# Kernel optimization log

Hardware: AMD Instinct MI355X
Metric: run time of the kernel (lower is better)

## Reference

```python
import jax, jax.numpy as jnp
import numpy as np

D_MODEL = 1024
D_STATE = 16
D_CONV = 4
EXPAND = 2
D_INNER = EXPAND * D_MODEL
DT_RANK = D_MODEL // 16  # ceil(1024/16) = 64
BSZ = 2
SEQ = 1024


def _silu(x):
    return x * jax.nn.sigmoid(x)


def _mamba(x, in_proj, conv_w, conv_b, x_proj, dt_w, dt_b, A_log, Dp, out_proj):
    """Single-direction Mamba block. x: (B, L, d_model)."""
    Bb, Ll, _ = x.shape
    xz = jnp.einsum('bld,ed->ble', x, in_proj)          # (B,L,2*d_inner)
    xi, z = jnp.split(xz, 2, axis=-1)                   # (B,L,d_inner)
    # depthwise causal conv1d over L (kernel d_conv)
    xp = jnp.pad(xi, ((0, 0), (D_CONV - 1, 0), (0, 0)))
    xc = conv_b + sum(conv_w[:, k] * xp[:, k:k + Ll, :] for k in range(D_CONV))
    xc = _silu(xc)                                      # (B,L,d_inner)
    dbl = jnp.einsum('ble,fe->blf', xc, x_proj)         # (B,L,dt_rank+2*d_state)
    dt, Bm, Cm = jnp.split(dbl, [DT_RANK, DT_RANK + D_STATE], axis=-1)
    delta = jax.nn.softplus(jnp.einsum('blr,er->ble', dt, dt_w) + dt_b)  # (B,L,d_inner)
    A = -jnp.exp(A_log)                                 # (d_inner,d_state)
    dA = jnp.exp(delta[..., None] * A)                  # (B,L,E,N)
    dBu = (delta * xc)[..., None] * Bm[:, :, None, :]   # (B,L,E,N)
    def step(h, t):
        dA_t, dBu_t, C_t = t
        h = dA_t * h + dBu_t                            # (B,E,N)
        return h, jnp.einsum('ben,bn->be', h, C_t)
    h0 = jnp.zeros((Bb, D_INNER, D_STATE), x.dtype)
    _, ys = jax.lax.scan(step, h0, (dA.transpose(1, 0, 2, 3),
                                    dBu.transpose(1, 0, 2, 3),
                                    Cm.transpose(1, 0, 2)))
    y = ys.transpose(1, 0, 2) + xc * Dp                 # skip connection
    y = y * _silu(z)                                    # gate
    return jnp.einsum('ble,de->bld', y, out_proj)


def setup_inputs() -> dict:
    key = jax.random.key(0)
    ks = jax.random.split(key, 4)
    def nrm(k, shape, s=0.02):
        return s * jax.random.normal(k, shape, dtype=jnp.float32)
    def mamba_params(kb):
        k = jax.random.split(kb, 6)
        return dict(
            in_proj=nrm(k[0], (2 * D_INNER, D_MODEL)),
            conv_w=nrm(k[1], (D_INNER, D_CONV), 0.2),
            conv_b=jnp.zeros((D_INNER,), jnp.float32),
            x_proj=nrm(k[2], (DT_RANK + 2 * D_STATE, D_INNER)),
            dt_w=nrm(k[3], (D_INNER, DT_RANK), 0.1),
            dt_b=nrm(k[4], (D_INNER,), 0.5) - 4.0,  # softplus -> dt ~ 0.018
            A_log=jnp.log(jnp.broadcast_to(jnp.arange(1, D_STATE + 1, dtype=jnp.float32), (D_INNER, D_STATE))),
            D=jnp.ones((D_INNER,), jnp.float32),
            out_proj=nrm(k[5], (D_MODEL, D_INNER)),
        )
    inp = {'x': jax.random.normal(ks[2], (BSZ, SEQ, D_MODEL), dtype=jnp.float32)}
    for name, p in (('fwd', mamba_params(ks[0])), ('bwd', mamba_params(ks[1]))):
        for kk, v in p.items():
            inp[f'{name}_{kk}'] = v
    inp['merge_w'] = nrm(ks[3], (D_MODEL, 2 * D_MODEL))
    return inp


def reference(x,
              fwd_in_proj, fwd_conv_w, fwd_conv_b, fwd_x_proj, fwd_dt_w, fwd_dt_b,
              fwd_A_log, fwd_D, fwd_out_proj,
              bwd_in_proj, bwd_conv_w, bwd_conv_b, bwd_x_proj, bwd_dt_w, bwd_dt_b,
              bwd_A_log, bwd_D, bwd_out_proj,
              merge_w):
    f = _mamba(x, fwd_in_proj, fwd_conv_w, fwd_conv_b, fwd_x_proj, fwd_dt_w,
               fwd_dt_b, fwd_A_log, fwd_D, fwd_out_proj)
    b = _mamba(jnp.flip(x, 1), bwd_in_proj, bwd_conv_w, bwd_conv_b, bwd_x_proj,
               bwd_dt_w, bwd_dt_b, bwd_A_log, bwd_D, bwd_out_proj)
    b = jnp.flip(b, 1)
    return jnp.einsum('blf,df->bld', jnp.concatenate([f, b], axis=-1), merge_w)
```

## Files before the change

kernel.cpp:

```cpp
#include <hip/hip_runtime.h>
#include <math.h>

#define BSZ 2
#define SEQ 1024
#define DM  1024
#define DI  2048
#define DS  16
#define DC  4
#define DR  64
#define NDBL 96
#define NC  32
#define LC  32
#define MM  (BSZ * SEQ)

typedef unsigned short u16;
typedef __bf16 bf16x8 __attribute__((ext_vector_type(8)));
typedef float  f32x4  __attribute__((ext_vector_type(4)));

constexpr int N4_X   = MM * DM / 4;
constexpr int N4_MW  = DM * 2 * DM / 4;
constexpr int N4_IN  = 2 * DI * DM / 4;
constexpr int N4_XP  = NDBL * DI / 4;
constexpr int N4_DT  = DI * DR / 4;
constexpr int N4_OUT = DM * DI / 4;
constexpr int N4_TOTAL = N4_X + N4_MW + 2 * (N4_IN + N4_XP + N4_DT + N4_OUT);
constexpr size_t O_XP  = (size_t)2 * DI * DM;
constexpr size_t O_DT  = O_XP + (size_t)NDBL * DI;
constexpr size_t O_OUT = O_DT + (size_t)DI * DR;
constexpr size_t WBF_SZ = O_OUT + (size_t)DM * DI;

__device__ __forceinline__ u16 f2b(float f) {
    unsigned int u = __float_as_uint(f);
    unsigned int r = (u + 0x7fffu + ((u >> 16) & 1u)) >> 16;
    return (u16)r;
}
__device__ __forceinline__ float b2f(u16 h) {
    return __uint_as_float(((unsigned int)h) << 16);
}

__device__ __forceinline__ void stf(float* p, size_t i, float v) { p[i] = v; }
__device__ __forceinline__ void stf(u16* p, size_t i, float v)   { p[i] = f2b(v); }

__device__ __forceinline__ float fexp(float x)  { return __expf(x); }
__device__ __forceinline__ float frcp(float x)  { return __builtin_amdgcn_rcpf(x); }
__device__ __forceinline__ float silu_fast(float x) {
    return x * frcp(1.f + fexp(-x));
}
__device__ __forceinline__ float softplus_fast(float x) {
    return (x > 15.f) ? x : __logf(1.f + fexp(x));
}

__device__ __forceinline__ void async16(const u16* g, u16* l) {
    __builtin_amdgcn_global_load_lds(
        (const __attribute__((address_space(1))) void*)g,
        (__attribute__((address_space(3))) void*)l, 16, 0, 0);
}

__device__ __forceinline__ int lds_slot(int row, int j) {
    return row * 4 + ((j + (row >> 1)) & 3);
}

__device__ __forceinline__ void stage8f(const float* p, u16* d) {
    float4 v0 = *(const float4*)p;
    float4 v1 = *(const float4*)(p + 4);
    ushort4 a; a.x = f2b(v0.x); a.y = f2b(v0.y); a.z = f2b(v0.z); a.w = f2b(v0.w);
    ushort4 b; b.x = f2b(v1.x); b.y = f2b(v1.y); b.z = f2b(v1.z); b.w = f2b(v1.w);
    *(ushort4*)d = a;
    *(ushort4*)(d + 4) = b;
}

__global__ __launch_bounds__(256) void cvt_all_kernel(
    const float* __restrict__ s0, const float* __restrict__ s1,
    const float* __restrict__ s2, const float* __restrict__ s3,
    const float* __restrict__ s4, const float* __restrict__ s5,
    const float* __restrict__ s6, const float* __restrict__ s7,
    const float* __restrict__ s8, const float* __restrict__ s9,
    u16* __restrict__ d0, u16* __restrict__ d1, u16* __restrict__ d2,
    u16* __restrict__ d3, u16* __restrict__ d4, u16* __restrict__ d5,
    u16* __restrict__ d6, u16* __restrict__ d7, u16* __restrict__ d8,
    u16* __restrict__ d9)
{
    int i = blockIdx.x * 256 + threadIdx.x;
    const float* s; u16* d;
    if (i < N4_X) { s = s0; d = d0; }
    else if ((i -= N4_X) < N4_MW) { s = s1; d = d1; }
    else if ((i -= N4_MW) < N4_IN) { s = s2; d = d2; }
    else if ((i -= N4_IN) < N4_XP) { s = s3; d = d3; }
    else if ((i -= N4_XP) < N4_DT) { s = s4; d = d4; }
    else if ((i -= N4_DT) < N4_OUT) { s = s5; d = d5; }
    else if ((i -= N4_OUT) < N4_IN) { s = s6; d = d6; }
    else if ((i -= N4_IN) < N4_XP) { s = s7; d = d7; }
    else if ((i -= N4_XP) < N4_DT) { s = s8; d = d8; }
    else if ((i -= N4_DT) < N4_OUT) { s = s9; d = d9; }
    else return;
    float4 v = ((const float4*)s)[i];
    ushort4 o; o.x = f2b(v.x); o.y = f2b(v.y); o.z = f2b(v.z); o.w = f2b(v.w);
    ((ushort4*)d)[i] = o;
}

template <typename TA, typename TC, int ACT, bool DUAL, bool FLIP1, int NSPLIT, int BN>
__global__ __launch_bounds__(256) void mfma_gemm(
    const TA* __restrict__ A0, const TA* __restrict__ A1, int lda,
    const u16* __restrict__ W0, const u16* __restrict__ W1, int ldw,
    const float* __restrict__ bias0, const float* __restrict__ bias1,
    TC* __restrict__ C0, TC* __restrict__ C1, int ldc,
    int M, int N, int K)
{
    constexpr int NF = BN / 32;
    __shared__ u16 As[128 * 32];
    __shared__ u16 Ws[BN * 32];

    const int z = blockIdx.z;
    const int dir = DUAL ? (z / NSPLIT) : 0;
    const int split = z % NSPLIT;
    const TA* A = dir ? A1 : A0;
    const u16* W = dir ? W1 : W0;
    const float* bias = dir ? bias1 : bias0;
    TC* C = dir ? C1 : C0;
    if (NSPLIT > 1) C += (size_t)split * M * ldc;
    const int kseg = K / NSPLIT;
    const int kbeg = split * kseg, kend = kbeg + kseg;

    const int t = threadIdx.x;
    const int wave = t >> 6;
    const int lane = t & 63;
    const int wm = (wave & 1) * 64;
    const int wn = (wave >> 1) * (BN / 2);
    const int fm = lane & 15;
    const int q  = lane >> 4;
    const int m0 = blockIdx.y * 128;
    const int n0 = blockIdx.x * BN;

    f32x4 acc[4][NF] = {};

    for (int k0 = kbeg; k0 < kend; k0 += 32) {
        if constexpr (__is_same(TA, u16)) {
            #pragma unroll
            for (int p = 0; p < 2; p++) {
                int i = p * 256 + wave * 64 + lane;
                int r = i >> 2;
                int j = ((i & 3) - (r >> 1)) & 3;
                async16(A + (size_t)(m0 + r) * lda + k0 + j * 8,
                        &As[(size_t)(p * 256 + wave * 64) * 8]);
            }
        } else {
            #pragma unroll
            for (int p = 0; p < 2; p++) {
                int i = p * 256 + t;
                int r = i >> 2;
                int j = ((i & 3) - (r >> 1)) & 3;
                stage8f(A + (size_t)(m0 + r) * lda + k0 + j * 8, &As[(size_t)i * 8]);
            }
        }
        #pragma unroll
        for (int p = 0; p < BN / 64; p++) {
            int i = p * 256 + wave * 64 + lane;
            int r = i >> 2;
            int j = ((i & 3) - (r >> 1)) & 3;
            int gr = n0 + r;
            if (gr >= N) gr = N - 1;
            async16(W + (size_t)gr * ldw + k0 + j * 8,
                    &Ws[(size_t)(p * 256 + wave * 64) * 8]);
        }
        __syncthreads();

        bf16x8 af[4], wf[NF];
        #pragma unroll
        for (int mi = 0; mi < 4; mi++)
            af[mi] = *(const bf16x8*)&As[(size_t)lds_slot(wm + mi * 16 + fm, q) * 8];
        #pragma unroll
        for (int ni = 0; ni < NF; ni++)
            wf[ni] = *(const bf16x8*)&Ws[(size_t)lds_slot(wn + ni * 16 + fm, q) * 8];
        #pragma unroll
        for (int mi = 0; mi < 4; mi++)
            #pragma unroll
            for (int ni = 0; ni < NF; ni++)
                acc[mi][ni] = __builtin_amdgcn_mfma_f32_16x16x32_bf16(
                    af[mi], wf[ni], acc[mi][ni], 0, 0, 0);
        __syncthreads();
    }

    const int rb = q * 4;
    const int cc = fm;
    #pragma unroll
    for (int mi = 0; mi < 4; mi++) {
        #pragma unroll
        for (int r = 0; r < 4; r++) {
            int gm = m0 + wm + mi * 16 + rb + r;
            int om = gm;
            if (FLIP1 && dir == 1) {
                int bb = gm / SEQ, l = gm % SEQ;
                om = bb * SEQ + (SEQ - 1 - l);
            }
            #pragma unroll
            for (int ni = 0; ni < NF; ni++) {
                int gn = n0 + wn + ni * 16 + cc;
                if (gn < N) {
                    float v = acc[mi][ni][r];
                    if (ACT == 1) v = softplus_fast(v + bias[gn]);
                    stf(C, (size_t)om * ldc + gn, v);
                }
            }
        }
    }
}

__global__ __launch_bounds__(256) void combine_dbl_kernel(
    const float* __restrict__ par, float* __restrict__ dbl)
{
    int i4 = blockIdx.x * 256 + threadIdx.x;
    const int per = (MM * NDBL) / 4;
    int dir = (i4 >= per) ? 1 : 0;
    int j4 = i4 - dir * per;
    const float* p = par + (size_t)dir * 4 * MM * NDBL;
    f32x4 s = {0.f, 0.f, 0.f, 0.f};
    #pragma unroll
    for (int k = 0; k < 4; k++)
        s += *(const f32x4*)&p[(size_t)k * MM * NDBL + (size_t)j4 * 4];
    *(f32x4*)&dbl[(size_t)dir * MM * NDBL + (size_t)j4 * 4] = s;
}

__global__ __launch_bounds__(256) void combine_cat_kernel(
    const float* __restrict__ par, u16* __restrict__ cat)
{
    int i4 = blockIdx.x * 256 + threadIdx.x;
    const int per = (MM * DM) / 4;
    int dir = (i4 >= per) ? 1 : 0;
    int j4 = i4 - dir * per;
    const float* p0 = par + (size_t)dir * 2 * MM * DM;
    const float* p1 = p0 + (size_t)MM * DM;
    f32x4 a = *(const f32x4*)&p0[(size_t)j4 * 4];
    f32x4 b = *(const f32x4*)&p1[(size_t)j4 * 4];
    int m = j4 >> 8;
    int n4 = j4 & 255;
    ushort4 o;
    o.x = f2b(a[0] + b[0]); o.y = f2b(a[1] + b[1]);
    o.z = f2b(a[2] + b[2]); o.w = f2b(a[3] + b[3]);
    *(ushort4*)&cat[(size_t)m * 2 * DM + dir * DM + n4 * 4] = o;
}

__global__ __launch_bounds__(256) void combine_out_kernel(
    const float* __restrict__ p0, float* __restrict__ out)
{
    int i4 = blockIdx.x * 256 + threadIdx.x;
    const float* p1 = p0 + (size_t)MM * DM;
    f32x4 a = *(const f32x4*)&p0[(size_t)i4 * 4];
    f32x4 b = *(const f32x4*)&p1[(size_t)i4 * 4];
    *(f32x4*)&out[(size_t)i4 * 4] = a + b;
}

__global__ __launch_bounds__(256) void conv_silu_kernel(
    const float* __restrict__ xz,
    const float* __restrict__ cw0, const float* __restrict__ cw1,
    const float* __restrict__ cb0, const float* __restrict__ cb1,
    u16* __restrict__ xcb)
{
    int i4 = blockIdx.x * 256 + threadIdx.x;
    const int per = MM * DI / 4;
    int dir = (i4 >= per) ? 1 : 0;
    int rem = i4 - dir * per;
    int e4 = rem & (DI / 4 - 1);
    int bl = rem / (DI / 4);
    int l = bl & (SEQ - 1);
    int e = e4 * 4;
    const float* xz_d = xz + (size_t)dir * MM * 2 * DI;
    const float* cw = dir ? cw1 : cw0;
    const float* cb = dir ? cb1 : cb0;
    f32x4 cwv[4];
    #pragma unroll
    for (int i = 0; i < 4; i++) cwv[i] = *(const f32x4*)&cw[(e + i) * DC];
    f32x4 acc = *(const f32x4*)&cb[e];
    #pragma unroll
    for (int k = 0; k < DC; k++) {
        int ll = l + k - (DC - 1);
        if (ll >= 0) {
            f32x4 xv = *(const f32x4*)&xz_d[(size_t)(bl - l + ll) * (2 * DI) + e];
            #pragma unroll
            for (int i = 0; i < 4; i++) acc[i] += cwv[i][k] * xv[i];
        }
    }
    ushort4 o;
    #pragma unroll
    for (int i = 0; i < 4; i++) {
        float s = silu_fast(acc[i]);
        ((u16*)&o)[i] = f2b(s);
    }
    ((ushort4*)xcb)[(size_t)dir * per + rem] = o;
}

__global__ __launch_bounds__(256) void scan_pass1(
    const float* __restrict__ dbl,
    const u16*  __restrict__ xc,
    const u16*  __restrict__ delta,
    const float* __restrict__ Alog0, const float* __restrict__ Alog1,
    float* __restrict__ Pout, float* __restrict__ Qout)
{
    __shared__ float sB[LC][16];
    const int t = threadIdx.x;
    const int c = blockIdx.x;
    const int dir = blockIdx.z >> 1;
    const int b = blockIdx.z & 1;
    const int e = blockIdx.y * 256 + t;
    const int row0 = b * SEQ + c * LC;
    const float* dbl_d = dbl + (size_t)dir * MM * NDBL;
    const u16* xc_d = xc + (size_t)dir * MM * DI;
    const u16* delta_d = delta + (size_t)dir * MM * DI;
    const float* A_log = dir ? Alog1 : Alog0;
    float* P_d = Pout + (size_t)dir * BSZ * NC * DI * DS;
    float* Q_d = Qout + (size_t)dir * BSZ * NC * DI * DS;

    if (t < LC * 4) {
        int row = t >> 2, col = (t & 3) * 4;
        *(f32x4*)&sB[row][col] =
            *(const f32x4*)&dbl_d[(size_t)(row0 + row) * NDBL + DR + col];
    }

    f32x4 Aen[4], P[4], Q[4];
    #pragma unroll
    for (int g = 0; g < 4; g++) {
        f32x4 a = *(const f32x4*)&A_log[(size_t)e * DS + g * 4];
        #pragma unroll
        for (int j = 0; j < 4; j++) Aen[g][j] = -fexp(a[j]);
        P[g] = f32x4{1.f, 1.f, 1.f, 1.f};
        Q[g] = f32x4{0.f, 0.f, 0.f, 0.f};
    }
    __syncthreads();

    float dv = b2f(delta_d[(size_t)row0 * DI + e]);
    float xv = b2f(xc_d[(size_t)row0 * DI + e]);
    for (int i = 0; i < LC; i++) {
        int ip = (i + 1 < LC) ? (i + 1) : (LC - 1);
        float dvn = b2f(delta_d[(size_t)(row0 + ip) * DI + e]);
        float xvn = b2f(xc_d[(size_t)(row0 + ip) * DI + e]);
        float du = dv * xv;
        #pragma unroll
        for (int g = 0; g < 4; g++) {
            f32x4 Bv = *(const f32x4*)&sB[i][g * 4];
            #pragma unroll
            for (int j = 0; j < 4; j++) {
                float dA = fexp(dv * Aen[g][j]);
                P[g][j] *= dA;
                Q[g][j] = dA * Q[g][j] + du * Bv[j];
            }
        }
        dv = dvn; xv = xvn;
    }
    size_t base = ((size_t)(b * NC + c) * DI + e) * DS;
    #pragma unroll
    for (int g = 0; g < 4; g++) {
        *(f32x4*)&P_d[base + g * 4] = P[g];
        *(f32x4*)&Q_d[base + g * 4] = Q[g];
    }
}

__global__ __launch_bounds__(256) void scan_pass2(
    const float* __restrict__ P, const float* __restrict__ Q,
    float* __restrict__ H0)
{
    const int gid = blockIdx.x * 256 + threadIdx.x;
    const int dir = gid >> 16;
    const int loc = gid & 65535;
    const int b = loc >> 15;
    const int en = loc & (DI * DS - 1);
    size_t doff = (size_t)dir * BSZ * NC * DI * DS;
    float h = 0.f;
    for (int c = 0; c < NC; c++) {
        size_t idx = doff + ((size_t)(b * NC + c) * DI * DS) + en;
        H0[idx] = h;
        h = P[idx] * h + Q[idx];
    }
}

__global__ __launch_bounds__(256) void scan_pass3(
    const float* __restrict__ dbl,
    const u16*  __restrict__ xc,
    const float* __restrict__ xz,
    u16* delta_y,
    const float* __restrict__ Alog0, const float* __restrict__ Alog1,
    const float* __restrict__ Dp0, const float* __restrict__ Dp1,
    const float* __restrict__ H0)
{
    __shared__ float sBC[LC][32];
    const int t = threadIdx.x;
    const int c = blockIdx.x;
    const int dir = blockIdx.z >> 1;
    const int b = blockIdx.z & 1;
    const int e = blockIdx.y * 256 + t;
    const int row0 = b * SEQ + c * LC;
    const float* dbl_d = dbl + (size_t)dir * MM * NDBL;
    const u16* xc_d = xc + (size_t)dir * MM * DI;
    const float* xz_d = xz + (size_t)dir * MM * 2 * DI;
    u16* dy_d = delta_y + (size_t)dir * MM * DI;
    const float* A_log = dir ? Alog1 : Alog0;
    const float* Dp = dir ? Dp1 : Dp0;
    const float* H0_d = H0 + (size_t)dir * BSZ * NC * DI * DS;

    {
        int row = t >> 3, col = (t & 7) * 4;
        *(f32x4*)&sBC[row][col] =
            *(const f32x4*)&dbl_d[(size_t)(row0 + row) * NDBL + DR + col];
    }

    f32x4 Aen[4], h[4];
    size_t base = ((size_t)(b * NC + c) * DI + e) * DS;
    #pragma unroll
    for (int g = 0; g < 4; g++) {
        f32x4 a = *(const f32x4*)&A_log[(size_t)e * DS + g * 4];
        #pragma unroll
        for (int j = 0; j < 4; j++) Aen[g][j] = -fexp(a[j]);
        h[g] = *(const f32x4*)&H0_d[base + g * 4];
    }
    const float Dv = Dp[e];
    __syncthreads();

    float dv = b2f(dy_d[(size_t)row0 * DI + e]);
    float xv = b2f(xc_d[(size_t)row0 * DI + e]);
    float zv = xz_d[(size_t)row0 * (2 * DI) + DI + e];
    for (int i = 0; i < LC; i++) {
        int ip = (i + 1 < LC) ? (i + 1) : (LC - 1);
        float dvn = b2f(dy_d[(size_t)(row0 + ip) * DI + e]);
        float xvn = b2f(xc_d[(size_t)(row0 + ip) * DI + e]);
        float zvn = xz_d[(size_t)(row0 + ip) * (2 * DI) + DI + e];
        float du = dv * xv;
        f32x4 pv = {0.f, 0.f, 0.f, 0.f};
        #pragma unroll
        for (int g = 0; g < 4; g++) {
            f32x4 Bv = *(const f32x4*)&sBC[i][g * 4];
            f32x4 Cv = *(const f32x4*)&sBC[i][16 + g * 4];
            #pragma unroll
            for (int j = 0; j < 4; j++) {
                float dA = fexp(dv * Aen[g][j]);
                h[g][j] = dA * h[g][j] + du * Bv[j];
                pv[j] += h[g][j] * Cv[j];
            }
        }
        float p = pv[0] + pv[1] + pv[2] + pv[3];
        float y = (p + xv * Dv) * silu_fast(zv);
        dy_d[(size_t)(row0 + i) * DI + e] = f2b(y);
        dv = dvn; xv = xvn; zv = zvn;
    }
}

extern "C" void kernel_launch(void* const* d_in, const int* in_sizes, int n_in,
                              void* d_out, int out_size, void* d_ws, size_t ws_size,
                              hipStream_t stream)
{
    const float* x = (const float*)d_in[0];
    const float* in_p[2]  = {(const float*)d_in[1],  (const float*)d_in[10]};
    const float* conv_w[2]= {(const float*)d_in[2],  (const float*)d_in[11]};
    const float* conv_b[2]= {(const float*)d_in[3],  (const float*)d_in[12]};
    const float* x_p[2]   = {(const float*)d_in[4],  (const float*)d_in[13]};
    const float* dt_w[2]  = {(const float*)d_in[5],  (const float*)d_in[14]};
    const float* dt_b[2]  = {(const float*)d_in[6],  (const float*)d_in[15]};
    const float* A_log[2] = {(const float*)d_in[7],  (const float*)d_in[16]};
    const float* Dp[2]    = {(const float*)d_in[8],  (const float*)d_in[17]};
    const float* out_p[2] = {(const float*)d_in[9],  (const float*)d_in[18]};
    const float* merge_w  = (const float*)d_in[19];
    float* out = (float*)d_out;

    float* ws = (float*)d_ws;
    float* ws_xz  = ws;
    float* ws_dbl = ws_xz  + (size_t)2 * MM * 2 * DI;
    float* ws_P   = ws_dbl + (size_t)2 * MM * NDBL;
    float* ws_Q   = ws_P   + (size_t)2 * BSZ * NC * DI * DS;
    float* ws_H0  = ws_Q   + (size_t)2 * BSZ * NC * DI * DS;
    u16* ws_delta = (u16*)(ws_H0 + (size_t)2 * BSZ * NC * DI * DS);
    u16* ws_xcb   = ws_delta + (size_t)2 * MM * DI;
    u16* ws_cat   = ws_xcb   + (size_t)2 * MM * DI;
    u16* ws_xbf   = ws_cat   + (size_t)MM * 2 * DM;
    u16* wbf_mw   = ws_xbf   + (size_t)MM * DM;
    u16* wbf0     = wbf_mw   + (size_t)DM * 2 * DM;
    u16* wbf1     = wbf0     + WBF_SZ;
    float* ws_par = ws_P;

    cvt_all_kernel<<<(N4_TOTAL + 255) / 256, 256, 0, stream>>>(
        x, merge_w, in_p[0], x_p[0], dt_w[0], out_p[0],
        in_p[1], x_p[1], dt_w[1], out_p[1],
        ws_xbf, wbf_mw,
        wbf0, wbf0 + O_XP, wbf0 + O_DT, wbf0 + O_OUT,
        wbf1, wbf1 + O_XP, wbf1 + O_DT, wbf1 + O_OUT);

    mfma_gemm<u16, float, 0, true, true, 1, 128><<<dim3(32, 16, 2), 256, 0, stream>>>(
        ws_xbf, ws_xbf, DM, wbf0, wbf1, DM, nullptr, nullptr,
        ws_xz, ws_xz + (size_t)MM * 2 * DI, 2 * DI, MM, 2 * DI, DM);

    conv_silu_kernel<<<(2 * MM * DI / 4) / 256, 256, 0, stream>>>(
        ws_xz, conv_w[0], conv_w[1], conv_b[0], conv_b[1], ws_xcb);

    mfma_gemm<u16, float, 0, true, false, 4, 64><<<dim3(2, 16, 8), 256, 0, stream>>>(
        ws_xcb, ws_xcb + (size_t)MM * DI, DI,
        wbf0 + O_XP, wbf1 + O_XP, DI, nullptr, nullptr,
        ws_par, ws_par + (size_t)4 * MM * NDBL, NDBL, MM, NDBL, DI);
    combine_dbl_kernel<<<(2 * MM * NDBL / 4) / 256, 256, 0, stream>>>(ws_par, ws_dbl);

    mfma_gemm<float, u16, 1, true, false, 1, 64><<<dim3(32, 16, 2), 256, 0, stream>>>(
        ws_dbl, ws_dbl + (size_t)MM * NDBL, NDBL,
        wbf0 + O_DT, wbf1 + O_DT, DR, dt_b[0], dt_b[1],
        ws_delta, ws_delta + (size_t)MM * DI, DI, MM, DI, DR);

    {
        dim3 grid(NC, DI / 256, 2 * BSZ);
        scan_pass1<<<grid, 256, 0, stream>>>(ws_dbl, ws_xcb, ws_delta,
                                             A_log[0], A_log[1], ws_P, ws_Q);
        scan_pass2<<<(2 * BSZ * DI * DS) / 256, 256, 0, stream>>>(ws_P, ws_Q, ws_H0);
        scan_pass3<<<grid, 256, 0, stream>>>(ws_dbl, ws_xcb, ws_xz, ws_delta,
                                             A_log[0], A_log[1], Dp[0], Dp[1], ws_H0);
    }

    mfma_gemm<u16, float, 0, true, true, 2, 64><<<dim3(16, 16, 4), 256, 0, stream>>>(
        ws_delta, ws_delta + (size_t)MM * DI, DI,
        wbf0 + O_OUT, wbf1 + O_OUT, DI, nullptr, nullptr,
        ws_par, ws_par + (size_t)2 * MM * DM, DM, MM, DM, DI);
    combine_cat_kernel<<<(2 * MM * DM / 4) / 256, 256, 0, stream>>>(ws_par, ws_cat);

    mfma_gemm<u16, float, 0, false, false, 2, 64><<<dim3(16, 16, 2), 256, 0, stream>>>(
        ws_cat, ws_cat, 2 * DM, wbf_mw, wbf_mw, 2 * DM, nullptr, nullptr,
        ws_par, ws_par, DM, MM, DM, 2 * DM);
    combine_out_kernel<<<(MM * DM / 4) / 256, 256, 0, stream>>>(ws_par, out);
}
```

Baseline: 395.8 us.

## Double-buffer GEMM LDS, swizzle XCDs, store xz in bf16, drop out-proj split-K

The GEMM kernel gets double-buffered LDS tiles so the next K-slice loads while MFMAs run, plus an optional XCD-aware block swizzle. The in_proj output xz is now stored as bf16 instead of fp32, which cuts traffic in conv and scan_pass3. The out-proj GEMM loses its split-K and writes bf16 directly into the concat buffer, so combine_cat is no longer needed. The scan chunk count changes from 32x32 to 16x64, which trades parallelism for fewer chunk carries. The extra bf16 rounding of xz and z may lower accuracy slightly.

```diff
diff --git a/kernel.cpp b/kernel.cpp
--- a/kernel.cpp
+++ b/kernel.cpp
@@ -9,8 +9,8 @@
 #define DC  4
 #define DR  64
 #define NDBL 96
-#define NC  32
-#define LC  32
+#define NC  16
+#define LC  64
 #define MM  (BSZ * SEQ)
 
 typedef unsigned short u16;
@@ -58,6 +58,12 @@
 
 __device__ __forceinline__ int lds_slot(int row, int j) {
     return row * 4 + ((j + (row >> 1)) & 3);
+}
+
+__device__ __forceinline__ int xcd_swz(int flat, int nwg) {
+    int q = nwg >> 3, r = nwg & 7;
+    int x = flat & 7, i = flat >> 3;
+    return (x < r ? x * (q + 1) : r * (q + 1) + (x - r) * q) + i;
 }
 
 __device__ __forceinline__ void stage8f(const float* p, u16* d) {
@@ -98,7 +104,8 @@
     ((ushort4*)d)[i] = o;
 }
 
-template <typename TA, typename TC, int ACT, bool DUAL, bool FLIP1, int NSPLIT, int BN>
+template <typename TA, typename TC, int ACT, bool DUAL, bool FLIP1, int NSPLIT,
+          int BN, bool SWZ>
 __global__ __launch_bounds__(256) void mfma_gemm(
     const TA* __restrict__ A0, const TA* __restrict__ A1, int lda,
     const u16* __restrict__ W0, const u16* __restrict__ W1, int ldw,
@@ -107,10 +114,22 @@
     int M, int N, int K)
 {
     constexpr int NF = BN / 32;
-    __shared__ u16 As[128 * 32];
-    __shared__ u16 Ws[BN * 32];
-
-    const int z = blockIdx.z;
+    __shared__ u16 As[2][128 * 32];
+    __shared__ u16 Ws[2][BN * 32];
+
+    int bx = blockIdx.x, by = blockIdx.y, bz = blockIdx.z;
+    if (SWZ) {
+        const int gx = gridDim.x, gy = gridDim.y;
+        const int nwg = gx * gy * gridDim.z;
+        int flat = (blockIdx.z * gy + blockIdx.y) * gx + blockIdx.x;
+        flat = xcd_swz(flat, nwg);
+        bx = flat % gx;
+        int rest = flat / gx;
+        by = rest % gy;
+        bz = rest / gy;
+    }
+
+    const int z = bz;
     const int dir = DUAL ? (z / NSPLIT) : 0;
     const int split = z % NSPLIT;
     const TA* A = dir ? A1 : A0;
@@ -119,7 +138,8 @@
     TC* C = dir ? C1 : C0;
     if (NSPLIT > 1) C += (size_t)split * M * ldc;
     const int kseg = K / NSPLIT;
-    const int kbeg = split * kseg, kend = kbeg + kseg;
+    const int kbeg = split * kseg;
+    const int kiters = kseg / 32;
 
     const int t = threadIdx.x;
     const int wave = t >> 6;
@@ -128,12 +148,10 @@
     const int wn = (wave >> 1) * (BN / 2);
     const int fm = lane & 15;
     const int q  = lane >> 4;
-    const int m0 = blockIdx.y * 128;
-    const int n0 = blockIdx.x * BN;
-
-    f32x4 acc[4][NF] = {};
-
-    for (int k0 = kbeg; k0 < kend; k0 += 32) {
+    const int m0 = by * 128;
+    const int n0 = bx * BN;
+
+    auto stage_tile = [&](int k0, int b) {
         if constexpr (__is_same(TA, u16)) {
             #pragma unroll
             for (int p = 0; p < 2; p++) {
@@ -141,7 +159,7 @@
                 int r = i >> 2;
                 int j = ((i & 3) - (r >> 1)) & 3;
                 async16(A + (size_t)(m0 + r) * lda + k0 + j * 8,
-                        &As[(size_t)(p * 256 + wave * 64) * 8]);
+                        &As[b][(size_t)(p * 256 + wave * 64) * 8]);
             }
         } else {
             #pragma unroll
@@ -149,7 +167,8 @@
                 int i = p * 256 + t;
                 int r = i >> 2;
                 int j = ((i & 3) - (r >> 1)) & 3;
-                stage8f(A + (size_t)(m0 + r) * lda + k0 + j * 8, &As[(size_t)i * 8]);
+                stage8f(A + (size_t)(m0 + r) * lda + k0 + j * 8,
+                        &As[b][(size_t)i * 8]);
             }
         }
         #pragma unroll
@@ -160,23 +179,36 @@
             int gr = n0 + r;
             if (gr >= N) gr = N - 1;
             async16(W + (size_t)gr * ldw + k0 + j * 8,
-                    &Ws[(size_t)(p * 256 + wave * 64) * 8]);
-        }
-        __syncthreads();
+                    &Ws[b][(size_t)(p * 256 + wave * 64) * 8]);
+        }
+    };
+
+    f32x4 acc[4][NF] = {};
+
+    stage_tile(kbeg, 0);
+    __syncthreads();
+
+    for (int ii = 0; ii < kiters; ii++) {
+        const int cur = ii & 1;
+        if (ii + 1 < kiters)
+            stage_tile(kbeg + (ii + 1) * 32, cur ^ 1);
 
         bf16x8 af[4], wf[NF];
         #pragma unroll
         for (int mi = 0; mi < 4; mi++)
-            af[mi] = *(const bf16x8*)&As[(size_t)lds_slot(wm + mi * 16 + fm, q) * 8];
+            af[mi] = *(const bf16x8*)
+                &As[cur][(size_t)lds_slot(wm + mi * 16 + fm, q) * 8];
         #pragma unroll
         for (int ni = 0; ni < NF; ni++)
-            wf[ni] = *(const bf16x8*)&Ws[(size_t)lds_slot(wn + ni * 16 + fm, q) * 8];
+            wf[ni] = *(const bf16x8*)
+                &Ws[cur][(size_t)lds_slot(wn + ni * 16 + fm, q) * 8];
         #pragma unroll
         for (int mi = 0; mi < 4; mi++)
             #pragma unroll
             for (int ni = 0; ni < NF; ni++)
                 acc[mi][ni] = __builtin_amdgcn_mfma_f32_16x16x32_bf16(
                     af[mi], wf[ni], acc[mi][ni], 0, 0, 0);
+
         __syncthreads();
     }
 
@@ -220,25 +252,6 @@
     *(f32x4*)&dbl[(size_t)dir * MM * NDBL + (size_t)j4 * 4] = s;
 }
 
-__global__ __launch_bounds__(256) void combine_cat_kernel(
-    const float* __restrict__ par, u16* __restrict__ cat)
-{
-    int i4 = blockIdx.x * 256 + threadIdx.x;
-    const int per = (MM * DM) / 4;
-    int dir = (i4 >= per) ? 1 : 0;
-    int j4 = i4 - dir * per;
-    const float* p0 = par + (size_t)dir * 2 * MM * DM;
-    const float* p1 = p0 + (size_t)MM * DM;
-    f32x4 a = *(const f32x4*)&p0[(size_t)j4 * 4];
-    f32x4 b = *(const f32x4*)&p1[(size_t)j4 * 4];
-    int m = j4 >> 8;
-    int n4 = j4 & 255;
-    ushort4 o;
-    o.x = f2b(a[0] + b[0]); o.y = f2b(a[1] + b[1]);
-    o.z = f2b(a[2] + b[2]); o.w = f2b(a[3] + b[3]);
-    *(ushort4*)&cat[(size_t)m * 2 * DM + dir * DM + n4 * 4] = o;
-}
-
 __global__ __launch_bounds__(256) void combine_out_kernel(
     const float* __restrict__ p0, float* __restrict__ out)
 {
@@ -250,7 +263,7 @@
 }
 
 __global__ __launch_bounds__(256) void conv_silu_kernel(
-    const float* __restrict__ xz,
+    const u16* __restrict__ xz,
     const float* __restrict__ cw0, const float* __restrict__ cw1,
     const float* __restrict__ cb0, const float* __restrict__ cb1,
     u16* __restrict__ xcb)
@@ -263,7 +276,7 @@
     int bl = rem / (DI / 4);
     int l = bl & (SEQ - 1);
     int e = e4 * 4;
-    const float* xz_d = xz + (size_t)dir * MM * 2 * DI;
+    const u16* xz_d = xz + (size_t)dir * MM * 2 * DI;
     const float* cw = dir ? cw1 : cw0;
     const float* cb = dir ? cb1 : cb0;
     f32x4 cwv[4];
@@ -274,9 +287,11 @@
     for (int k = 0; k < DC; k++) {
         int ll = l + k - (DC - 1);
         if (ll >= 0) {
-            f32x4 xv = *(const f32x4*)&xz_d[(size_t)(bl - l + ll) * (2 * DI) + e];
-            #pragma unroll
-            for (int i = 0; i < 4; i++) acc[i] += cwv[i][k] * xv[i];
+            ushort4 xv = *(const ushort4*)&xz_d[(size_t)(bl - l + ll) * (2 * DI) + e];
+            acc[0] += cwv[0][k] * b2f(xv.x);
+            acc[1] += cwv[1][k] * b2f(xv.y);
+            acc[2] += cwv[2][k] * b2f(xv.z);
+            acc[3] += cwv[3][k] * b2f(xv.w);
         }
     }
     ushort4 o;
@@ -309,10 +324,14 @@
     float* P_d = Pout + (size_t)dir * BSZ * NC * DI * DS;
     float* Q_d = Qout + (size_t)dir * BSZ * NC * DI * DS;
 
-    if (t < LC * 4) {
-        int row = t >> 2, col = (t & 3) * 4;
-        *(f32x4*)&sB[row][col] =
-            *(const f32x4*)&dbl_d[(size_t)(row0 + row) * NDBL + DR + col];
+    #pragma unroll
+    for (int it = 0; it < (LC * 4 + 255) / 256; it++) {
+        int idx = it * 256 + t;
+        if (idx < LC * 4) {
+            int row = idx >> 2, col = (idx & 3) * 4;
+            *(f32x4*)&sB[row][col] =
+                *(const f32x4*)&dbl_d[(size_t)(row0 + row) * NDBL + DR + col];
+        }
     }
 
     f32x4 Aen[4], P[4], Q[4];
@@ -374,7 +393,7 @@
 __global__ __launch_bounds__(256) void scan_pass3(
     const float* __restrict__ dbl,
     const u16*  __restrict__ xc,
-    const float* __restrict__ xz,
+    const u16*  __restrict__ xz,
     u16* delta_y,
     const float* __restrict__ Alog0, const float* __restrict__ Alog1,
     const float* __restrict__ Dp0, const float* __restrict__ Dp1,
@@ -389,14 +408,15 @@
     const int row0 = b * SEQ + c * LC;
     const float* dbl_d = dbl + (size_t)dir * MM * NDBL;
     const u16* xc_d = xc + (size_t)dir * MM * DI;
-    const float* xz_d = xz + (size_t)dir * MM * 2 * DI;
+    const u16* xz_d = xz + (size_t)dir * MM * 2 * DI;
     u16* dy_d = delta_y + (size_t)dir * MM * DI;
     const float* A_log = dir ? Alog1 : Alog0;
     const float* Dp = dir ? Dp1 : Dp0;
     const float* H0_d = H0 + (size_t)dir * BSZ * NC * DI * DS;
 
-    {
-        int row = t >> 3, col = (t & 7) * 4;
+    #pragma unroll
+    for (int it = 0; it < LC / 32; it++) {
+        int row = it * 32 + (t >> 3), col = (t & 7) * 4;
         *(f32x4*)&sBC[row][col] =
             *(const f32x4*)&dbl_d[(size_t)(row0 + row) * NDBL + DR + col];
     }
@@ -415,12 +435,12 @@
 
     float dv = b2f(dy_d[(size_t)row0 * DI + e]);
     float xv = b2f(xc_d[(size_t)row0 * DI + e]);
-    float zv = xz_d[(size_t)row0 * (2 * DI) + DI + e];
+    float zv = b2f(xz_d[(size_t)row0 * (2 * DI) + DI + e]);
     for (int i = 0; i < LC; i++) {
         int ip = (i + 1 < LC) ? (i + 1) : (LC - 1);
         float dvn = b2f(dy_d[(size_t)(row0 + ip) * DI + e]);
         float xvn = b2f(xc_d[(size_t)(row0 + ip) * DI + e]);
-        float zvn = xz_d[(size_t)(row0 + ip) * (2 * DI) + DI + e];
+        float zvn = b2f(xz_d[(size_t)(row0 + ip) * (2 * DI) + DI + e]);
         float du = dv * xv;
         f32x4 pv = {0.f, 0.f, 0.f, 0.f};
         #pragma unroll
@@ -459,12 +479,12 @@
     float* out = (float*)d_out;
 
     float* ws = (float*)d_ws;
-    float* ws_xz  = ws;
-    float* ws_dbl = ws_xz  + (size_t)2 * MM * 2 * DI;
+    float* ws_dbl = ws;
     float* ws_P   = ws_dbl + (size_t)2 * MM * NDBL;
     float* ws_Q   = ws_P   + (size_t)2 * BSZ * NC * DI * DS;
     float* ws_H0  = ws_Q   + (size_t)2 * BSZ * NC * DI * DS;
-    u16* ws_delta = (u16*)(ws_H0 + (size_t)2 * BSZ * NC * DI * DS);
+    u16* ws_xz    = (u16*)(ws_H0 + (size_t)2 * BSZ * NC * DI * DS);
+    u16* ws_delta = ws_xz    + (size_t)2 * MM * 2 * DI;
     u16* ws_xcb   = ws_delta + (size_t)2 * MM * DI;
     u16* ws_cat   = ws_xcb   + (size_t)2 * MM * DI;
     u16* ws_xbf   = ws_cat   + (size_t)MM * 2 * DM;
@@ -480,20 +500,23 @@
         wbf0, wbf0 + O_XP, wbf0 + O_DT, wbf0 + O_OUT,
         wbf1, wbf1 + O_XP, wbf1 + O_DT, wbf1 + O_OUT);
 
-    mfma_gemm<u16, float, 0, true, true, 1, 128><<<dim3(32, 16, 2), 256, 0, stream>>>(
+    mfma_gemm<u16, u16, 0, true, true, 1, 128, true>
+        <<<dim3(32, 16, 2), 256, 0, stream>>>(
         ws_xbf, ws_xbf, DM, wbf0, wbf1, DM, nullptr, nullptr,
         ws_xz, ws_xz + (size_t)MM * 2 * DI, 2 * DI, MM, 2 * DI, DM);
 
     conv_silu_kernel<<<(2 * MM * DI / 4) / 256, 256, 0, stream>>>(
         ws_xz, conv_w[0], conv_w[1], conv_b[0], conv_b[1], ws_xcb);
 
-    mfma_gemm<u16, float, 0, true, false, 4, 64><<<dim3(2, 16, 8), 256, 0, stream>>>(
+    mfma_gemm<u16, float, 0, true, false, 4, 64, true>
+        <<<dim3(2, 16, 8), 256, 0, stream>>>(
         ws_xcb, ws_xcb + (size_t)MM * DI, DI,
         wbf0 + O_XP, wbf1 + O_XP, DI, nullptr, nullptr,
         ws_par, ws_par + (size_t)4 * MM * NDBL, NDBL, MM, NDBL, DI);
     combine_dbl_kernel<<<(2 * MM * NDBL / 4) / 256, 256, 0, stream>>>(ws_par, ws_dbl);
 
-    mfma_gemm<float, u16, 1, true, false, 1, 64><<<dim3(32, 16, 2), 256, 0, stream>>>(
+    mfma_gemm<float, u16, 1, true, false, 1, 64, true>
+        <<<dim3(32, 16, 2), 256, 0, stream>>>(
         ws_dbl, ws_dbl + (size_t)MM * NDBL, NDBL,
         wbf0 + O_DT, wbf1 + O_DT, DR, dt_b[0], dt_b[1],
         ws_delta, ws_delta + (size_t)MM * DI, DI, MM, DI, DR);
@@ -507,13 +530,14 @@
                                              A_log[0], A_log[1], Dp[0], Dp[1], ws_H0);
     }
 
-    mfma_gemm<u16, float, 0, true, true, 2, 64><<<dim3(16, 16, 4), 256, 0, stream>>>(
+    mfma_gemm<u16, u16, 0, true, true, 1, 64, true>
+        <<<dim3(16, 16, 2), 256, 0, stream>>>(
         ws_delta, ws_delta + (size_t)MM * DI, DI,
         wbf0 + O_OUT, wbf1 + O_OUT, DI, nullptr, nullptr,
-        ws_par, ws_par + (size_t)2 * MM * DM, DM, MM, DM, DI);
-    combine_cat_kernel<<<(2 * MM * DM / 4) / 256, 256, 0, stream>>>(ws_par, ws_cat);
-
-    mfma_gemm<u16, float, 0, false, false, 2, 64><<<dim3(16, 16, 2), 256, 0, stream>>>(
+        ws_cat, ws_cat + DM, 2 * DM, MM, DM, DI);
+
+    mfma_gemm<u16, float, 0, false, false, 2, 64, true>
+        <<<dim3(16, 16, 2), 256, 0, stream>>>(
         ws_cat, ws_cat, 2 * DM, wbf_mw, wbf_mw, 2 * DM, nullptr, nullptr,
         ws_par, ws_par, DM, MM, DM, 2 * DM);
     combine_out_kernel<<<(MM * DM / 4) / 256, 256, 0, stream>>>(ws_par, out);
```

Result: faster. 378.7 us (-4.3%).
